# Kernel optimization log

Hardware: AMD Instinct MI355X
Metric: run time of the kernel (lower is better)

Reference implementation:

```python
import jax, jax.numpy as jnp
import numpy as np

EMBED_DIM = 1024
NUM_HEADS = 16
HEAD_DIM = EMBED_DIM // NUM_HEADS
SCALE_BASE = EMBED_DIM  # XPOS(head_dim, embed_dim): embed_dim is scale_base
BSZ, SEQ = 8, 1024


def xpos_apply(x, downscale):
    # x: [B*H, L, D]; standard xpos (torchscale) rotary with position-dependent scale
    L, D = x.shape[1], x.shape[2]
    half = D // 2
    s = (jnp.arange(0, D, 2, dtype=jnp.float32) + 0.4 * D) / (1.4 * D)  # [half]
    min_pos = -(L // 2)  # offset = 0
    pos = jnp.arange(min_pos, min_pos + L, dtype=jnp.float32)  # [L]
    scale = s[None, :] ** (pos[:, None] / SCALE_BASE)  # [L, half]
    inv_freq = 1.0 / (10000.0 ** (jnp.arange(half, dtype=jnp.float32) / half))
    sinus = jnp.arange(L, dtype=jnp.float32)[:, None] * inv_freq[None, :]  # [L, half]
    sin, cos = jnp.sin(sinus), jnp.cos(sinus)
    if downscale:
        scale = 1.0 / scale
    # duplicate_interleave: repeat each column twice -> [L, D]
    sin_d = jnp.repeat(sin * scale, 2, axis=-1)
    cos_d = jnp.repeat(cos * scale, 2, axis=-1)
    x1, x2 = x[..., 0::2], x[..., 1::2]
    rot = jnp.stack([-x2, x1], axis=-1).reshape(x.shape)  # rotate_every_two
    return x * cos_d + rot * sin_d


def setup_inputs() -> dict:
    key = jax.random.key(0)
    ks = jax.random.split(key, 12)
    std = 0.02
    inp = {
        'query': jax.random.normal(ks[0], (BSZ, SEQ, EMBED_DIM), jnp.float32),
        'key': jax.random.normal(ks[1], (BSZ, SEQ, EMBED_DIM), jnp.float32),
        'value': jax.random.normal(ks[2], (BSZ, SEQ, EMBED_DIM), jnp.float32),
        'wq': jax.random.normal(ks[3], (EMBED_DIM, EMBED_DIM), jnp.float32) * std,
        'bq': jax.random.normal(ks[4], (EMBED_DIM,), jnp.float32) * std,
        'wk': jax.random.normal(ks[5], (EMBED_DIM, EMBED_DIM), jnp.float32) * std,
        'bk': jax.random.normal(ks[6], (EMBED_DIM,), jnp.float32) * std,
        'wv': jax.random.normal(ks[7], (EMBED_DIM, EMBED_DIM), jnp.float32) * std,
        'bv': jax.random.normal(ks[8], (EMBED_DIM,), jnp.float32) * std,
        'wo': jax.random.normal(ks[9], (EMBED_DIM, EMBED_DIM), jnp.float32) * std,
        'bo': jax.random.normal(ks[10], (EMBED_DIM,), jnp.float32) * std,
    }
    return inp


def reference(query, key, value, wq, bq, wk, bk, wv, bv, wo, bo):
    B, T, E = query.shape
    S = key.shape[1]
    scaling = HEAD_DIM ** -0.5
    q = (query @ wq.T + bq) * scaling
    k = key @ wk.T + bk
    v = value @ wv.T + bv

    def split_heads(x, L):
        return x.reshape(B, L, NUM_HEADS, HEAD_DIM).transpose(0, 2, 1, 3).reshape(B * NUM_HEADS, L, HEAD_DIM)

    q = split_heads(q, T)
    k = split_heads(k, S)
    v = split_heads(v, S)
    k = xpos_apply(k, downscale=True)
    q = xpos_apply(q, downscale=False)
    attn_w = jnp.einsum('btd,bsd->bts', q, k)  # [B*H, T, S]
    attn_w = jax.nn.softmax(attn_w.astype(jnp.float32), axis=-1).astype(q.dtype)
    attn = jnp.einsum('bts,bsd->btd', attn_w, v)  # [B*H, T, D]
    attn = attn.reshape(B, NUM_HEADS, T, HEAD_DIM).transpose(0, 2, 1, 3).reshape(B, T, E)
    return attn @ wo.T + bo
```

## Files before the change

### kernel.cpp

```cpp
#include <hip/hip_runtime.h>


#define BSZ  8
#define SEQ  1024
#define EMB  1024
#define NH   16
#define HD   64
#define HALF 32
#define BH   (BSZ*NH)
#define MROWS (BSZ*SEQ)

typedef __attribute__((ext_vector_type(4))) float f32x4;
typedef __attribute__((ext_vector_type(8))) short bf16x8;

__device__ __forceinline__ ushort f2bf(float f) {
    union { float f; unsigned u; } v; v.f = f;
    return (ushort)((v.u + 0x7FFFu + ((v.u >> 16) & 1u)) >> 16);
}

__device__ __forceinline__ unsigned cvt_pk_bf16(float a, float b) {
    unsigned r;
    asm("v_cvt_pk_bf16_f32 %0, %1, %2" : "=v"(r) : "v"(a), "v"(b));
    return r;
}

__device__ __forceinline__ void async16(void* lds, const void* g) {
    __builtin_amdgcn_global_load_lds(
        (const __attribute__((address_space(1))) unsigned int*)g,
        (__attribute__((address_space(3))) unsigned int*)lds, 16, 0, 0);
}

__global__ __launch_bounds__(256)
void castw_kernel(const float* __restrict__ w0, const float* __restrict__ w1,
                  const float* __restrict__ w2, const float* __restrict__ w3,
                  ushort* __restrict__ d0, ushort* __restrict__ d1,
                  ushort* __restrict__ d2, ushort* __restrict__ d3, int n4) {
    int i = blockIdx.x * 256 + threadIdx.x;
    if (i >= n4) return;
    const float* s = blockIdx.y == 0 ? w0 : blockIdx.y == 1 ? w1
                   : blockIdx.y == 2 ? w2 : w3;
    ushort* d = blockIdx.y == 0 ? d0 : blockIdx.y == 1 ? d1
              : blockIdx.y == 2 ? d2 : d3;
    float4 v = reinterpret_cast<const float4*>(s)[i];
    ushort4 o;
    o.x = f2bf(v.x); o.y = f2bf(v.y); o.z = f2bf(v.z); o.w = f2bf(v.w);
    reinterpret_cast<ushort4*>(d)[i] = o;
}

__global__ __launch_bounds__(256)
void xpos_tables_kernel(float* __restrict__ tab) {
    int idx = blockIdx.x * 256 + threadIdx.x;
    if (idx >= SEQ * HALF) return;
    int t = idx >> 5;
    int j = idx & 31;
    float s        = (2.0f * (float)j + 0.4f * (float)HD) / (1.4f * (float)HD);
    float pos      = (float)(t - SEQ / 2);
    float scale    = powf(s, pos * (1.0f / 1024.0f));
    float inv_freq = powf(10000.0f, -(float)j / (float)HALF);
    float ang      = (float)t * inv_freq;
    float sn = sinf(ang), cs = cosf(ang);
    float inv_scale = 1.0f / scale;
    tab[0 * SEQ * HALF + idx] = sn * scale;
    tab[1 * SEQ * HALF + idx] = cs * scale;
    tab[2 * SEQ * HALF + idx] = sn * inv_scale;
    tab[3 * SEQ * HALF + idx] = cs * inv_scale;
}

__global__ __launch_bounds__(256)
void qkv_gemm_kernel(const float* __restrict__ Aq, const float* __restrict__ Ak,
                     const float* __restrict__ Av,
                     const ushort* __restrict__ Wq, const ushort* __restrict__ Wk,
                     const ushort* __restrict__ Wv,
                     const float* __restrict__ bq, const float* __restrict__ bk,
                     const float* __restrict__ bv,
                     const float* __restrict__ tab,
                     ushort* __restrict__ oq, ushort* __restrict__ ok,
                     ushort* __restrict__ ov) {
    __shared__ ushort As[2][128 * 64];
    __shared__ ushort Bs[2][128 * 64];
    const int ymode = blockIdx.y;
    const float*  A    = ymode == 0 ? Aq : ymode == 1 ? Ak : Av;
    const ushort* W    = ymode == 0 ? Wq : ymode == 1 ? Wk : Wv;
    const float*  bias = ymode == 0 ? bq : ymode == 1 ? bk : bv;
    ushort*       outp = ymode == 0 ? oq : ymode == 1 ? ok : ov;

    const int tid  = threadIdx.x;
    const int lane = tid & 63;
    const int w    = tid >> 6;
    const int g    = lane >> 4;
    const int c    = lane & 15;
    const int wr   = w >> 1, wc = w & 1;

    int lid = blockIdx.x;
    int wg  = (lid & 7) * 64 + (lid >> 3);
    const int row0 = (wg >> 3) * 128;
    const int col0 = (wg & 7) * 128;

    f32x4 acc[4][4] = {};

    const int ar  = tid >> 1;
    const int ach = (tid & 1) * 32;
    const int asw = (ar & 7) << 4;
    const float4* abase4 =
        reinterpret_cast<const float4*>(A + (size_t)(row0 + ar) * EMB) + (ach >> 2);

    int srow[4], scol[4];
    #pragma unroll
    for (int i = 0; i < 4; ++i) {
        int f = i * 4096 + tid * 16;
        int r = f >> 7, cb = f & 127;
        srow[i] = r;
        scol[i] = (cb ^ ((r & 7) << 4)) >> 1;
    }

    auto stageB = [&](int buf, int k0) {
        #pragma unroll
        for (int i = 0; i < 4; ++i)
            async16(&Bs[buf][i * 2048 + w * 512],
                    &W[(size_t)(col0 + srow[i]) * EMB + k0 + scol[i]]);
    };
    auto writeA = [&](int buf, const float4* av) {
        #pragma unroll
        for (int a = 0; a < 4; ++a) {
            const float* pf = reinterpret_cast<const float*>(&av[2 * a]);
            uint4 u;
            u.x = cvt_pk_bf16(pf[0], pf[1]);
            u.y = cvt_pk_bf16(pf[2], pf[3]);
            u.z = cvt_pk_bf16(pf[4], pf[5]);
            u.w = cvt_pk_bf16(pf[6], pf[7]);
            *reinterpret_cast<uint4*>(
                reinterpret_cast<char*>(&As[buf][0]) + ar * 128 +
                ((2 * (ach + 8 * a)) ^ asw)) = u;
        }
    };

    float4 av[8];
    #pragma unroll
    for (int i = 0; i < 8; ++i) av[i] = abase4[i];
    writeA(0, av);
    stageB(0, 0);
    __syncthreads();

    for (int t = 0; t < 16; ++t) {
        const int cur = t & 1;
        if (t < 15) {
            #pragma unroll
            for (int i = 0; i < 8; ++i) av[i] = abase4[(t + 1) * 16 + i];
            stageB(cur ^ 1, (t + 1) * 64);
        }

        const char* abase = reinterpret_cast<const char*>(&As[cur][0]);
        const char* bbase = reinterpret_cast<const char*>(&Bs[cur][0]);
        #pragma unroll
        for (int ks = 0; ks < 2; ++ks) {
            bf16x8 af[4], bfr[4];
            #pragma unroll
            for (int mi = 0; mi < 4; ++mi) {
                int r = wr * 64 + mi * 16 + c;
                af[mi] = *reinterpret_cast<const bf16x8*>(
                    abase + r * 128 + ((ks * 64 + g * 16) ^ ((r & 7) << 4)));
            }
            #pragma unroll
            for (int ni = 0; ni < 4; ++ni) {
                int r = wc * 64 + ni * 16 + c;
                bfr[ni] = *reinterpret_cast<const bf16x8*>(
                    bbase + r * 128 + ((ks * 64 + g * 16) ^ ((r & 7) << 4)));
            }
            #pragma unroll
            for (int mi = 0; mi < 4; ++mi)
                #pragma unroll
                for (int ni = 0; ni < 4; ++ni)
                    acc[mi][ni] = __builtin_amdgcn_mfma_f32_16x16x32_bf16(
                        af[mi], bfr[ni], acc[mi][ni], 0, 0, 0);
        }

        if (t < 15) writeA(cur ^ 1, av);
        __syncthreads();
    }

    #pragma unroll
    for (int ni = 0; ni < 4; ++ni) {
        int n = col0 + wc * 64 + ni * 16 + c;
        float bn = bias[n];
        #pragma unroll
        for (int mi = 0; mi < 4; ++mi) {
            #pragma unroll
            for (int r = 0; r < 4; ++r) {
                int m = row0 + wr * 64 + mi * 16 + g * 4 + r;
                float val = acc[mi][ni][r] + bn;
                if (ymode == 0) val *= 0.125f;
                if (ymode != 2) {
                    int t = m & (SEQ - 1);
                    int d = n & 63;
                    const int base = (ymode == 0 ? 0 : 2) * SEQ * HALF + t * HALF;
                    float sn = tab[base + (d >> 1)];
                    float cs = tab[base + SEQ * HALF + (d >> 1)];
                    float other = __shfl_xor(val, 1);
                    val = val * cs + ((d & 1) ? other * sn : -other * sn);
                }
                int b = m >> 10, t2 = m & 1023;
                int h = n >> 6,  d2 = n & 63;
                outp[(((size_t)b * NH + h) * SEQ + t2) * HD + d2] = f2bf(val);
            }
        }
    }
}

template <int MODE>
__global__ __launch_bounds__(256)
void gemm_bf16_kernel(const ushort* __restrict__ A, const ushort* __restrict__ W,
                      const float* __restrict__ bias, const float* __restrict__ tab,
                      void* __restrict__ outp) {
    __shared__ ushort As[2][128 * 64];
    __shared__ ushort Bs[2][128 * 64];
    const int tid  = threadIdx.x;
    const int lane = tid & 63;
    const int w    = tid >> 6;
    const int g    = lane >> 4;
    const int c    = lane & 15;
    const int wr   = w >> 1, wc = w & 1;

    int lid = blockIdx.x;
    int wg  = (lid & 7) * 64 + (lid >> 3);
    const int row0 = (wg >> 3) * 128;
    const int col0 = (wg & 7) * 128;

    f32x4 acc[4][4] = {};

    int srow[4], scol[4];
    #pragma unroll
    for (int i = 0; i < 4; ++i) {
        int f = i * 4096 + tid * 16;
        int r = f >> 7, cb = f & 127;
        srow[i] = r;
        scol[i] = (cb ^ ((r & 7) << 4)) >> 1;
    }

    auto stage = [&](int buf, int k0) {
        #pragma unroll
        for (int i = 0; i < 4; ++i) {
            const ushort* srcA;
            if (MODE == 3) {
                int h = k0 >> 6;
                srcA = &A[(((size_t)(row0 >> 10) * NH + h) * SEQ +
                           (row0 & 1023) + srow[i]) * HD + scol[i]];
            } else {
                srcA = &A[(size_t)(row0 + srow[i]) * EMB + k0 + scol[i]];
            }
            async16(&As[buf][i * 2048 + w * 512], srcA);
        }
        #pragma unroll
        for (int i = 0; i < 4; ++i)
            async16(&Bs[buf][i * 2048 + w * 512],
                    &W[(size_t)(col0 + srow[i]) * EMB + k0 + scol[i]]);
    };

    stage(0, 0);
    __syncthreads();

    for (int t = 0; t < 16; ++t) {
        const int cur = t & 1;
        if (t < 15) stage(cur ^ 1, (t + 1) * 64);

        const char* abase = reinterpret_cast<const char*>(&As[cur][0]);
        const char* bbase = reinterpret_cast<const char*>(&Bs[cur][0]);
        #pragma unroll
        for (int ks = 0; ks < 2; ++ks) {
            bf16x8 af[4], bfr[4];
            #pragma unroll
            for (int mi = 0; mi < 4; ++mi) {
                int r = wr * 64 + mi * 16 + c;
                af[mi] = *reinterpret_cast<const bf16x8*>(
                    abase + r * 128 + ((ks * 64 + g * 16) ^ ((r & 7) << 4)));
            }
            #pragma unroll
            for (int ni = 0; ni < 4; ++ni) {
                int r = wc * 64 + ni * 16 + c;
                bfr[ni] = *reinterpret_cast<const bf16x8*>(
                    bbase + r * 128 + ((ks * 64 + g * 16) ^ ((r & 7) << 4)));
            }
            #pragma unroll
            for (int mi = 0; mi < 4; ++mi)
                #pragma unroll
                for (int ni = 0; ni < 4; ++ni)
                    acc[mi][ni] = __builtin_amdgcn_mfma_f32_16x16x32_bf16(
                        af[mi], bfr[ni], acc[mi][ni], 0, 0, 0);
        }
        __syncthreads();
    }

    #pragma unroll
    for (int ni = 0; ni < 4; ++ni) {
        int n = col0 + wc * 64 + ni * 16 + c;
        float bn = bias[n];
        #pragma unroll
        for (int mi = 0; mi < 4; ++mi) {
            #pragma unroll
            for (int r = 0; r < 4; ++r) {
                int m = row0 + wr * 64 + mi * 16 + g * 4 + r;
                float val = acc[mi][ni][r] + bn;
                if (MODE == 3) {
                    ((float*)outp)[(size_t)m * EMB + n] = val;
                } else {
                    int b = m >> 10, t = m & 1023;
                    int h = n >> 6,  d = n & 63;
                    ((ushort*)outp)[(((size_t)b * NH + h) * SEQ + t) * HD + d] =
                        f2bf(val);
                }
            }
        }
    }
}

__global__ __launch_bounds__(256)
void vtrans_kernel(const ushort* __restrict__ v, ushort* __restrict__ vt) {
    __shared__ ushort T[64][72];
    const int tid = threadIdx.x;
    const int bh  = blockIdx.y;
    const int t0  = blockIdx.x * 64;
    const ushort* vb = &v[((size_t)bh * SEQ + t0) * HD];
    #pragma unroll
    for (int p = 0; p < 2; ++p) {
        int chunk = p * 256 + tid;
        int tl = chunk >> 3;
        int d8 = (chunk & 7) * 8;
        ushort tmp[8];
        *reinterpret_cast<uint4*>(tmp) =
            *reinterpret_cast<const uint4*>(&vb[tl * HD + d8]);
        #pragma unroll
        for (int j = 0; j < 8; ++j) T[d8 + j][tl] = tmp[j];
    }
    __syncthreads();
    ushort* ob = &vt[(size_t)bh * HD * SEQ + t0];
    #pragma unroll
    for (int p = 0; p < 2; ++p) {
        int chunk = p * 256 + tid;
        int dl = chunk >> 3;
        int t8 = (chunk & 7) * 8;
        *reinterpret_cast<uint4*>(&ob[(size_t)dl * SEQ + t8]) =
            *reinterpret_cast<const uint4*>(&T[dl][t8]);
    }
}

__global__ __launch_bounds__(256)
void attn_kernel(const ushort* __restrict__ qg, const ushort* __restrict__ kg,
                 const ushort* __restrict__ vtg, ushort* __restrict__ og) {
    __shared__ ushort Ks[2 * 4096];
    __shared__ ushort Vs[2 * 4096];
    __shared__ ushort Ps[4096];
    const int tid  = threadIdx.x;
    const int lane = tid & 63;
    const int w    = tid >> 6;
    const int g    = lane >> 4;
    const int c    = lane & 15;

    int lid = blockIdx.x;
    int wg  = (lid & 7) * 256 + (lid >> 3);
    const int bh = wg >> 4;
    const int q0 = (wg & 15) * 64;

    const ushort* qrow = &qg[((size_t)bh * SEQ + q0 + w * 16 + c) * HD];
    bf16x8 qf[2];
    qf[0] = *reinterpret_cast<const bf16x8*>(qrow + g * 8);
    qf[1] = *reinterpret_cast<const bf16x8*>(qrow + 32 + g * 8);

    float m_run[4], l_part[4];
    f32x4 oacc[4] = {};
    #pragma unroll
    for (int r = 0; r < 4; ++r) { m_run[r] = -1e30f; l_part[r] = 0.f; }

    int srow[2], scol[2];
    #pragma unroll
    for (int i = 0; i < 2; ++i) {
        int f = i * 4096 + tid * 16;
        int r = f >> 7, cb = f & 127;
        srow[i] = r; scol[i] = (cb ^ ((r & 7) << 4)) >> 1;
    }

    const ushort* kb  = &kg[(size_t)bh * SEQ * HD];
    const ushort* vtb = &vtg[(size_t)bh * HD * SEQ];

    auto stage = [&](int buf, int kt) {
        #pragma unroll
        for (int i = 0; i < 2; ++i) {
            async16(&Ks[buf * 4096 + i * 2048 + w * 512],
                    &kb[(size_t)(kt + srow[i]) * HD + scol[i]]);
            async16(&Vs[buf * 4096 + i * 2048 + w * 512],
                    &vtb[(size_t)srow[i] * SEQ + kt + scol[i]]);
        }
    };

    stage(0, 0);
    __syncthreads();

    char* pbase = reinterpret_cast<char*>(Ps) + w * 2048;

    for (int kt = 0; kt < SEQ; kt += 64) {
        const int cur = (kt >> 6) & 1;
        if (kt + 64 < SEQ) stage(cur ^ 1, kt + 64);

        const char* kbase = reinterpret_cast<const char*>(Ks) + cur * 8192;
        const char* vbase = reinterpret_cast<const char*>(Vs) + cur * 8192;

        f32x4 s[4];
        #pragma unroll
        for (int j = 0; j < 4; ++j) {
            int key = j * 16 + c;
            int sw  = (key & 7) << 4;
            f32x4 a = {};
            #pragma unroll
            for (int ks = 0; ks < 2; ++ks) {
                bf16x8 kf = *reinterpret_cast<const bf16x8*>(
                    kbase + key * 128 + ((ks * 64 + g * 16) ^ sw));
                a = __builtin_amdgcn_mfma_f32_16x16x32_bf16(qf[ks], kf, a, 0, 0, 0);
            }
            s[j] = a;
        }

        float pmax[4];
        #pragma unroll
        for (int r = 0; r < 4; ++r)
            pmax[r] = fmaxf(fmaxf(s[0][r], s[1][r]), fmaxf(s[2][r], s[3][r]));
        int need = (pmax[0] > m_run[0] + 8.f) || (pmax[1] > m_run[1] + 8.f) ||
                   (pmax[2] > m_run[2] + 8.f) || (pmax[3] > m_run[3] + 8.f);
        if (__any(need)) {
            #pragma unroll
            for (int r = 0; r < 4; ++r) {
                float mx = pmax[r];
                mx = fmaxf(mx, __shfl_xor(mx, 1));
                mx = fmaxf(mx, __shfl_xor(mx, 2));
                mx = fmaxf(mx, __shfl_xor(mx, 4));
                mx = fmaxf(mx, __shfl_xor(mx, 8));
                float mn = fmaxf(m_run[r], mx);
                float alpha = __expf(m_run[r] - mn);
                l_part[r] *= alpha;
                #pragma unroll
                for (int dblk = 0; dblk < 4; ++dblk) oacc[dblk][r] *= alpha;
                m_run[r] = mn;
            }
        }

        #pragma unroll
        for (int r = 0; r < 4; ++r) {
            int q  = g * 4 + r;
            int sw = (q & 7) << 4;
            char* pq = pbase + q * 128;
            float p0 = __expf(s[0][r] - m_run[r]);
            float p1 = __expf(s[1][r] - m_run[r]);
            float p2 = __expf(s[2][r] - m_run[r]);
            float p3 = __expf(s[3][r] - m_run[r]);
            l_part[r] += (p0 + p1) + (p2 + p3);
            unsigned pk01 = cvt_pk_bf16(p0, p1);
            unsigned pk23 = cvt_pk_bf16(p2, p3);
            *reinterpret_cast<ushort*>(pq + (( 0 + 2 * c) ^ sw)) = (ushort)pk01;
            *reinterpret_cast<ushort*>(pq + ((32 + 2 * c) ^ sw)) = (ushort)(pk01 >> 16);
            *reinterpret_cast<ushort*>(pq + ((64 + 2 * c) ^ sw)) = (ushort)pk23;
            *reinterpret_cast<ushort*>(pq + ((96 + 2 * c) ^ sw)) = (ushort)(pk23 >> 16);
        }

        #pragma unroll
        for (int ks = 0; ks < 2; ++ks) {
            bf16x8 pf = *reinterpret_cast<const bf16x8*>(
                pbase + c * 128 + ((ks * 64 + g * 16) ^ ((c & 7) << 4)));
            #pragma unroll
            for (int dblk = 0; dblk < 4; ++dblk) {
                int d = dblk * 16 + c;
                bf16x8 vf = *reinterpret_cast<const bf16x8*>(
                    vbase + d * 128 + ((ks * 64 + g * 16) ^ ((d & 7) << 4)));
                oacc[dblk] = __builtin_amdgcn_mfma_f32_16x16x32_bf16(
                    pf, vf, oacc[dblk], 0, 0, 0);
            }
        }
        __syncthreads();
    }

    #pragma unroll
    for (int r = 0; r < 4; ++r) {
        float rs = l_part[r];
        rs += __shfl_xor(rs, 1);
        rs += __shfl_xor(rs, 2);
        rs += __shfl_xor(rs, 4);
        rs += __shfl_xor(rs, 8);
        float inv = 1.f / rs;
        int q = q0 + w * 16 + g * 4 + r;
        #pragma unroll
        for (int dblk = 0; dblk < 4; ++dblk)
            og[((size_t)bh * SEQ + q) * HD + dblk * 16 + c] =
                f2bf(oacc[dblk][r] * inv);
    }
}

extern "C" void kernel_launch(void* const* d_in, const int* in_sizes, int n_in,
                              void* d_out, int out_size, void* d_ws,
                              size_t ws_size, hipStream_t stream) {
    const float* query = (const float*)d_in[0];
    const float* key_  = (const float*)d_in[1];
    const float* value = (const float*)d_in[2];
    const float* wq    = (const float*)d_in[3];
    const float* bq    = (const float*)d_in[4];
    const float* wk    = (const float*)d_in[5];
    const float* bk    = (const float*)d_in[6];
    const float* wv    = (const float*)d_in[7];
    const float* bv    = (const float*)d_in[8];
    const float* wo    = (const float*)d_in[9];
    const float* bo    = (const float*)d_in[10];

    ushort* ws16 = (ushort*)d_ws;
    const size_t NX = (size_t)MROWS * EMB;
    const size_t NW = (size_t)EMB * EMB;
    ushort* wqb = ws16;
    ushort* wkb = wqb + NW;
    ushort* wvb = wkb + NW;
    ushort* wob = wvb + NW;
    float*  tab = (float*)(wob + NW);
    ushort* qb  = (ushort*)(tab + 4 * SEQ * HALF);
    ushort* kb  = qb + NX;
    ushort* vb  = kb + NX;
    ushort* vt  = vb + NX;
    ushort* ob  = vt + NX;

    const int nw4 = (int)(NW / 4);

    castw_kernel<<<dim3(nw4 / 256, 4), 256, 0, stream>>>(
        wq, wk, wv, wo, wqb, wkb, wvb, wob, nw4);
    xpos_tables_kernel<<<SEQ * HALF / 256, 256, 0, stream>>>(tab);

    qkv_gemm_kernel<<<dim3(512, 3), 256, 0, stream>>>(
        query, key_, value, wqb, wkb, wvb, bq, bk, bv, tab, qb, kb, vb);

    vtrans_kernel<<<dim3(16, 128), 256, 0, stream>>>(vb, vt);

    attn_kernel<<<2048, 256, 0, stream>>>(qb, kb, vt, ob);

    gemm_bf16_kernel<3><<<512, 256, 0, stream>>>(ob, wob, bo, nullptr,
                                                 (float*)d_out);
}
```

Measured before the change: 410.1 us.

## Single-buffer QKV GEMM with fp32 LDS staging and widen attention blocks to 512 threads

The QKV projection GEMM now stages fp32 activations straight into shared memory with async copies and converts them to bf16 at fragment-load time. It drops the register-prefetched double buffer for a single buffer and asks for 3 blocks per CU. The attention kernel moves to 512-thread blocks that each cover 128 queries, so every K/V tile is reused by twice as many waves, with one async copy per thread. Softmax P stores go back to scalar f2bf conversion. Single buffering exposes load latency in the GEMM, and fp32 staging doubles LDS traffic for A.

```diff
diff --git a/kernel.cpp b/kernel.cpp
--- a/kernel.cpp
+++ b/kernel.cpp
@@ -66,7 +66,7 @@
     tab[3 * SEQ * HALF + idx] = cs * inv_scale;
 }
 
-__global__ __launch_bounds__(256)
+__global__ __launch_bounds__(256, 3)
 void qkv_gemm_kernel(const float* __restrict__ Aq, const float* __restrict__ Ak,
                      const float* __restrict__ Av,
                      const ushort* __restrict__ Wq, const ushort* __restrict__ Wk,
@@ -76,8 +76,8 @@
                      const float* __restrict__ tab,
                      ushort* __restrict__ oq, ushort* __restrict__ ok,
                      ushort* __restrict__ ov) {
-    __shared__ ushort As[2][128 * 64];
-    __shared__ ushort Bs[2][128 * 64];
+    __shared__ float  Asf[128 * 64];
+    __shared__ ushort Bs[128 * 64];
     const int ymode = blockIdx.y;
     const float*  A    = ymode == 0 ? Aq : ymode == 1 ? Ak : Av;
     const ushort* W    = ymode == 0 ? Wq : ymode == 1 ? Wk : Wv;
@@ -98,73 +98,58 @@
 
     f32x4 acc[4][4] = {};
 
-    const int ar  = tid >> 1;
-    const int ach = (tid & 1) * 32;
-    const int asw = (ar & 7) << 4;
-    const float4* abase4 =
-        reinterpret_cast<const float4*>(A + (size_t)(row0 + ar) * EMB) + (ach >> 2);
-
-    int srow[4], scol[4];
+    int arow[8], acol[8];
+    #pragma unroll
+    for (int i = 0; i < 8; ++i) {
+        int f = i * 4096 + tid * 16;
+        int r = f >> 8, pb = f & 255;
+        arow[i] = r;
+        acol[i] = (pb ^ ((r & 7) << 5)) >> 2;
+    }
+    int brow[4], bcol[4];
     #pragma unroll
     for (int i = 0; i < 4; ++i) {
         int f = i * 4096 + tid * 16;
         int r = f >> 7, cb = f & 127;
-        srow[i] = r;
-        scol[i] = (cb ^ ((r & 7) << 4)) >> 1;
-    }
-
-    auto stageB = [&](int buf, int k0) {
+        brow[i] = r;
+        bcol[i] = (cb ^ ((r & 7) << 4)) >> 1;
+    }
+
+    for (int t = 0; t < 16; ++t) {
+        const int k0 = t * 64;
+        #pragma unroll
+        for (int i = 0; i < 8; ++i)
+            async16(&Asf[i * 1024 + w * 256],
+                    &A[(size_t)(row0 + arow[i]) * EMB + k0 + acol[i]]);
         #pragma unroll
         for (int i = 0; i < 4; ++i)
-            async16(&Bs[buf][i * 2048 + w * 512],
-                    &W[(size_t)(col0 + srow[i]) * EMB + k0 + scol[i]]);
-    };
-    auto writeA = [&](int buf, const float4* av) {
-        #pragma unroll
-        for (int a = 0; a < 4; ++a) {
-            const float* pf = reinterpret_cast<const float*>(&av[2 * a]);
-            uint4 u;
-            u.x = cvt_pk_bf16(pf[0], pf[1]);
-            u.y = cvt_pk_bf16(pf[2], pf[3]);
-            u.z = cvt_pk_bf16(pf[4], pf[5]);
-            u.w = cvt_pk_bf16(pf[6], pf[7]);
-            *reinterpret_cast<uint4*>(
-                reinterpret_cast<char*>(&As[buf][0]) + ar * 128 +
-                ((2 * (ach + 8 * a)) ^ asw)) = u;
-        }
-    };
-
-    float4 av[8];
-    #pragma unroll
-    for (int i = 0; i < 8; ++i) av[i] = abase4[i];
-    writeA(0, av);
-    stageB(0, 0);
-    __syncthreads();
-
-    for (int t = 0; t < 16; ++t) {
-        const int cur = t & 1;
-        if (t < 15) {
-            #pragma unroll
-            for (int i = 0; i < 8; ++i) av[i] = abase4[(t + 1) * 16 + i];
-            stageB(cur ^ 1, (t + 1) * 64);
-        }
-
-        const char* abase = reinterpret_cast<const char*>(&As[cur][0]);
-        const char* bbase = reinterpret_cast<const char*>(&Bs[cur][0]);
+            async16(&Bs[i * 2048 + w * 512],
+                    &W[(size_t)(col0 + brow[i]) * EMB + k0 + bcol[i]]);
+        __syncthreads();
+
         #pragma unroll
         for (int ks = 0; ks < 2; ++ks) {
             bf16x8 af[4], bfr[4];
             #pragma unroll
             for (int mi = 0; mi < 4; ++mi) {
-                int r = wr * 64 + mi * 16 + c;
-                af[mi] = *reinterpret_cast<const bf16x8*>(
-                    abase + r * 128 + ((ks * 64 + g * 16) ^ ((r & 7) << 4)));
+                int r  = wr * 64 + mi * 16 + c;
+                int pb = (ks * 128 + g * 32) ^ ((r & 7) << 5);
+                const char* ab = reinterpret_cast<const char*>(Asf) + r * 256 + pb;
+                f32x4 a0 = *reinterpret_cast<const f32x4*>(ab);
+                f32x4 a1 = *reinterpret_cast<const f32x4*>(ab + 16);
+                union { uint4 u; bf16x8 v; } pk;
+                pk.u.x = cvt_pk_bf16(a0[0], a0[1]);
+                pk.u.y = cvt_pk_bf16(a0[2], a0[3]);
+                pk.u.z = cvt_pk_bf16(a1[0], a1[1]);
+                pk.u.w = cvt_pk_bf16(a1[2], a1[3]);
+                af[mi] = pk.v;
             }
             #pragma unroll
             for (int ni = 0; ni < 4; ++ni) {
                 int r = wc * 64 + ni * 16 + c;
                 bfr[ni] = *reinterpret_cast<const bf16x8*>(
-                    bbase + r * 128 + ((ks * 64 + g * 16) ^ ((r & 7) << 4)));
+                    reinterpret_cast<const char*>(Bs) + r * 128 +
+                    ((ks * 64 + g * 16) ^ ((r & 7) << 4)));
             }
             #pragma unroll
             for (int mi = 0; mi < 4; ++mi)
@@ -173,8 +158,6 @@
                     acc[mi][ni] = __builtin_amdgcn_mfma_f32_16x16x32_bf16(
                         af[mi], bfr[ni], acc[mi][ni], 0, 0, 0);
         }
-
-        if (t < 15) writeA(cur ^ 1, av);
         __syncthreads();
     }
 
@@ -190,17 +173,17 @@
                 float val = acc[mi][ni][r] + bn;
                 if (ymode == 0) val *= 0.125f;
                 if (ymode != 2) {
-                    int t = m & (SEQ - 1);
-                    int d = n & 63;
-                    const int base = (ymode == 0 ? 0 : 2) * SEQ * HALF + t * HALF;
+                    int t2 = m & (SEQ - 1);
+                    int d  = n & 63;
+                    const int base = (ymode == 0 ? 0 : 2) * SEQ * HALF + t2 * HALF;
                     float sn = tab[base + (d >> 1)];
                     float cs = tab[base + SEQ * HALF + (d >> 1)];
                     float other = __shfl_xor(val, 1);
                     val = val * cs + ((d & 1) ? other * sn : -other * sn);
                 }
-                int b = m >> 10, t2 = m & 1023;
+                int b = m >> 10, t3 = m & 1023;
                 int h = n >> 6,  d2 = n & 63;
-                outp[(((size_t)b * NH + h) * SEQ + t2) * HD + d2] = f2bf(val);
+                outp[(((size_t)b * NH + h) * SEQ + t3) * HD + d2] = f2bf(val);
             }
         }
     }
@@ -302,9 +285,9 @@
                 if (MODE == 3) {
                     ((float*)outp)[(size_t)m * EMB + n] = val;
                 } else {
-                    int b = m >> 10, t = m & 1023;
+                    int b = m >> 10, t2 = m & 1023;
                     int h = n >> 6,  d = n & 63;
-                    ((ushort*)outp)[(((size_t)b * NH + h) * SEQ + t) * HD + d] =
+                    ((ushort*)outp)[(((size_t)b * NH + h) * SEQ + t2) * HD + d] =
                         f2bf(val);
                 }
             }
@@ -342,12 +325,12 @@
     }
 }
 
-__global__ __launch_bounds__(256)
+__global__ __launch_bounds__(512, 6)
 void attn_kernel(const ushort* __restrict__ qg, const ushort* __restrict__ kg,
                  const ushort* __restrict__ vtg, ushort* __restrict__ og) {
     __shared__ ushort Ks[2 * 4096];
     __shared__ ushort Vs[2 * 4096];
-    __shared__ ushort Ps[4096];
+    __shared__ ushort Ps[8 * 1024];
     const int tid  = threadIdx.x;
     const int lane = tid & 63;
     const int w    = tid >> 6;
@@ -355,9 +338,9 @@
     const int c    = lane & 15;
 
     int lid = blockIdx.x;
-    int wg  = (lid & 7) * 256 + (lid >> 3);
-    const int bh = wg >> 4;
-    const int q0 = (wg & 15) * 64;
+    int wg  = (lid & 7) * 128 + (lid >> 3);
+    const int bh = wg >> 3;
+    const int q0 = (wg & 7) * 128;
 
     const ushort* qrow = &qg[((size_t)bh * SEQ + q0 + w * 16 + c) * HD];
     bf16x8 qf[2];
@@ -369,25 +352,18 @@
     #pragma unroll
     for (int r = 0; r < 4; ++r) { m_run[r] = -1e30f; l_part[r] = 0.f; }
 
-    int srow[2], scol[2];
-    #pragma unroll
-    for (int i = 0; i < 2; ++i) {
-        int f = i * 4096 + tid * 16;
-        int r = f >> 7, cb = f & 127;
-        srow[i] = r; scol[i] = (cb ^ ((r & 7) << 4)) >> 1;
-    }
+    const int sf   = tid * 16;
+    const int srow = sf >> 7;
+    const int scol = ((sf & 127) ^ ((srow & 7) << 4)) >> 1;
 
     const ushort* kb  = &kg[(size_t)bh * SEQ * HD];
     const ushort* vtb = &vtg[(size_t)bh * HD * SEQ];
 
     auto stage = [&](int buf, int kt) {
-        #pragma unroll
-        for (int i = 0; i < 2; ++i) {
-            async16(&Ks[buf * 4096 + i * 2048 + w * 512],
-                    &kb[(size_t)(kt + srow[i]) * HD + scol[i]]);
-            async16(&Vs[buf * 4096 + i * 2048 + w * 512],
-                    &vtb[(size_t)srow[i] * SEQ + kt + scol[i]]);
-        }
+        async16(&Ks[buf * 4096 + w * 512],
+                &kb[(size_t)(kt + srow) * HD + scol]);
+        async16(&Vs[buf * 4096 + w * 512],
+                &vtb[(size_t)srow * SEQ + kt + scol]);
     };
 
     stage(0, 0);
@@ -444,18 +420,13 @@
         for (int r = 0; r < 4; ++r) {
             int q  = g * 4 + r;
             int sw = (q & 7) << 4;
-            char* pq = pbase + q * 128;
-            float p0 = __expf(s[0][r] - m_run[r]);
-            float p1 = __expf(s[1][r] - m_run[r]);
-            float p2 = __expf(s[2][r] - m_run[r]);
-            float p3 = __expf(s[3][r] - m_run[r]);
-            l_part[r] += (p0 + p1) + (p2 + p3);
-            unsigned pk01 = cvt_pk_bf16(p0, p1);
-            unsigned pk23 = cvt_pk_bf16(p2, p3);
-            *reinterpret_cast<ushort*>(pq + (( 0 + 2 * c) ^ sw)) = (ushort)pk01;
-            *reinterpret_cast<ushort*>(pq + ((32 + 2 * c) ^ sw)) = (ushort)(pk01 >> 16);
-            *reinterpret_cast<ushort*>(pq + ((64 + 2 * c) ^ sw)) = (ushort)pk23;
-            *reinterpret_cast<ushort*>(pq + ((96 + 2 * c) ^ sw)) = (ushort)(pk23 >> 16);
+            #pragma unroll
+            for (int j = 0; j < 4; ++j) {
+                float p = __expf(s[j][r] - m_run[r]);
+                l_part[r] += p;
+                int byt = q * 128 + (((j * 16 + c) * 2) ^ sw);
+                *reinterpret_cast<ushort*>(pbase + byt) = f2bf(p);
+            }
         }
 
         #pragma unroll
@@ -530,7 +501,7 @@
 
     vtrans_kernel<<<dim3(16, 128), 256, 0, stream>>>(vb, vt);
 
-    attn_kernel<<<2048, 256, 0, stream>>>(qb, kb, vt, ob);
+    attn_kernel<<<1024, 512, 0, stream>>>(qb, kb, vt, ob);
 
     gemm_bf16_kernel<3><<<512, 256, 0, stream>>>(ob, wob, bo, nullptr,
                                                  (float*)d_out);
```

Measured after the change: 377.6 us. 1.09x faster.
